# Performance work log

Hardware: AMD Instinct MI355X
Metric: run time of the kernel (lower is better)

Reference implementation:

```python
import jax, jax.numpy as jnp
import numpy as np

WS = 8            # window_size
N = WS * WS       # tokens per window = 64
C = 512           # dim
TEMB = 512        # temb_dim
H = 8             # num_heads
D = C // H        # head_dim = 64
B = 2048          # number of windows (batch * windows per image)


def _rel_pos_index(ws: int) -> np.ndarray:
    coords = np.stack(np.meshgrid(np.arange(ws), np.arange(ws), indexing='ij'))  # (2, ws, ws)
    flat = coords.reshape(2, -1)                      # (2, N)
    rel = flat[:, :, None] - flat[:, None, :]         # (2, N, N)
    rel = rel.transpose(1, 2, 0).copy()               # (N, N, 2)
    rel[:, :, 0] += ws - 1
    rel[:, :, 1] += ws - 1
    rel[:, :, 0] *= 2 * ws - 1
    return rel.sum(-1)                                # (N, N) int

_RP_INDEX = jnp.asarray(_rel_pos_index(WS))           # (N, N)


def setup_inputs() -> dict:
    key = jax.random.key(0)
    ks = jax.random.split(key, 8)
    std = 0.02
    return {
        'x': jax.random.normal(ks[0], (B, N, C), dtype=jnp.float32),
        'temb': jax.random.normal(ks[1], (B, TEMB), dtype=jnp.float32),
        'w_qkv': jax.random.normal(ks[2], (C, 3 * C), dtype=jnp.float32) * std,
        'b_qkv': jnp.zeros((3 * C,), dtype=jnp.float32),
        'w_qkv_t': jax.random.normal(ks[3], (TEMB, 3 * C), dtype=jnp.float32) * std,
        'w_proj': jax.random.normal(ks[4], (C, C), dtype=jnp.float32) * std,
        'b_proj': jnp.zeros((C,), dtype=jnp.float32),
        'rpb_table': jax.random.normal(ks[5], ((2 * WS - 1) ** 2, H), dtype=jnp.float32) * std,
    }


def reference(x, temb, w_qkv, b_qkv, w_qkv_t, w_proj, b_proj, rpb_table):
    # x: (B, N, C), temb: (B, TEMB)
    scale = D ** (-0.5)
    qkv = x @ w_qkv + b_qkv + (temb @ w_qkv_t)[:, None, :]     # (B, N, 3C)
    qkv = qkv.reshape(x.shape[0], N, 3, H, D)
    q = qkv[:, :, 0].transpose(0, 2, 1, 3)                      # (B, H, N, D)
    k = qkv[:, :, 1].transpose(0, 2, 1, 3)
    v = qkv[:, :, 2].transpose(0, 2, 1, 3)
    attn = jnp.einsum('bhnd,bhmd->bhnm', q * scale, k)          # (B, H, N, N)
    bias = rpb_table[_RP_INDEX]                                 # (N, N, H)
    attn = attn + bias.transpose(2, 0, 1)[None]                 # + (1, H, N, N)
    attn = jax.nn.softmax(attn, axis=-1)
    out = jnp.einsum('bhnm,bhmd->bhnd', attn, v)                # (B, H, N, D)
    out = out.transpose(0, 2, 1, 3).reshape(x.shape[0], N, C)   # (B, N, C)
    return out @ w_proj + b_proj
```

## Files before the change

### kernel.cpp

```cpp
#include <hip/hip_runtime.h>

typedef __bf16 bf16;
typedef __bf16 bf16x4 __attribute__((ext_vector_type(4)));
typedef __bf16 bf16x8 __attribute__((ext_vector_type(8)));
typedef float f32x4 __attribute__((ext_vector_type(4)));

#define MFMA(a, b, c) __builtin_amdgcn_mfma_f32_16x16x32_bf16((a), (b), (c), 0, 0, 0)

__global__ void transpose_cast(const float* __restrict__ in, bf16* __restrict__ out,
                               int R, int C) {
  int i = blockIdx.x * 256 + threadIdx.x;
  if (i >= R * C) return;
  int r = i / C, c = i - r * C;
  out[(size_t)c * R + r] = (bf16)in[i];
}

template <bool AF32>
__global__ __launch_bounds__(256) void gemm_bt_bias(
    const void* __restrict__ Ap, const bf16* __restrict__ Bt,
    const float* __restrict__ bias, float* __restrict__ C,
    int M, int N, int K) {
  __shared__ bf16 lA[128 * 32];
  __shared__ bf16 lB[128 * 32];
  const int t = threadIdx.x, l = t & 63;
  const int w = t >> 6, wr = w >> 1, wc = w & 1;
  const int li = l & 15, kl = (l >> 4) << 3;
  const long bm0 = (long)blockIdx.x * 128, bn0 = (long)blockIdx.y * 128;
  f32x4 acc[4][4] = {};
  for (int ks = 0; ks < (K >> 5); ++ks) {
    const int k0 = ks << 5;
    __syncthreads();
#pragma unroll
    for (int i = 0; i < 2; ++i) {
      int u = t + (i << 8);
      int row = u >> 2, kc = (u & 3) << 3;
      if constexpr (AF32) {
        const float* ag = (const float*)Ap + (bm0 + row) * K + k0 + kc;
        f32x4 v0 = *((const f32x4*)ag);
        f32x4 v1 = *((const f32x4*)(ag + 4));
        bf16x8 pk;
        pk[0] = (bf16)v0[0]; pk[1] = (bf16)v0[1]; pk[2] = (bf16)v0[2]; pk[3] = (bf16)v0[3];
        pk[4] = (bf16)v1[0]; pk[5] = (bf16)v1[1]; pk[6] = (bf16)v1[2]; pk[7] = (bf16)v1[3];
        *((bf16x8*)&lA[u << 3]) = pk;
      } else {
        *((bf16x8*)&lA[u << 3]) =
            *((const bf16x8*)((const bf16*)Ap + (bm0 + row) * K + k0 + kc));
      }
      *((bf16x8*)&lB[u << 3]) = *((const bf16x8*)&Bt[(bn0 + row) * K + k0 + kc]);
    }
    __syncthreads();
    bf16x8 af[4], bfr[4];
#pragma unroll
    for (int mt = 0; mt < 4; ++mt)
      af[mt] = *((const bf16x8*)&lA[(wr * 64 + mt * 16 + li) * 32 + kl]);
#pragma unroll
    for (int nt = 0; nt < 4; ++nt)
      bfr[nt] = *((const bf16x8*)&lB[(wc * 64 + nt * 16 + li) * 32 + kl]);
#pragma unroll
    for (int mt = 0; mt < 4; ++mt)
#pragma unroll
      for (int nt = 0; nt < 4; ++nt)
        acc[mt][nt] = MFMA(af[mt], bfr[nt], acc[mt][nt]);
  }
#pragma unroll
  for (int mt = 0; mt < 4; ++mt)
#pragma unroll
    for (int nt = 0; nt < 4; ++nt) {
      long col = bn0 + wc * 64 + nt * 16 + li;
      float bv = bias[col];
#pragma unroll
      for (int r = 0; r < 4; ++r) {
        long row = bm0 + wr * 64 + mt * 16 + ((l >> 4) << 2) + r;
        C[row * N + col] = acc[mt][nt][r] + bv;
      }
    }
}

__global__ __launch_bounds__(256) void fused_qkv_attn(
    const float* __restrict__ x, const bf16* __restrict__ w1t,
    const float* __restrict__ tbias, const float* __restrict__ rpb,
    bf16* __restrict__ attn_out) {
  __shared__ bf16 xs[64 * 520];
  __shared__ float ts[1536];
  __shared__ bf16 qs[64 * 72];
  __shared__ bf16 kts[64 * 72];
  __shared__ bf16 vts[64 * 72];
  __shared__ bf16 ps[64 * 72];

  const int b = blockIdx.x;
  const int t = threadIdx.x, l = t & 63, w = t >> 6;
  const int li = l & 15, lg = l >> 4, kl = lg << 3;

  {
    const float* xb = x + (size_t)b * (64 * 512);
#pragma unroll
    for (int i = 0; i < 32; ++i) {
      int f4 = t + (i << 8);
      int n = f4 >> 7, c4 = (f4 & 127) << 2;
      f32x4 v = *((const f32x4*)&xb[n * 512 + c4]);
      bf16x4 pk;
      pk[0] = (bf16)v[0]; pk[1] = (bf16)v[1]; pk[2] = (bf16)v[2]; pk[3] = (bf16)v[3];
      *((bf16x4*)&xs[n * 520 + c4]) = pk;
    }
    const float* tb = tbias + (size_t)b * 1536;
    for (int i = t; i < 1536; i += 256) ts[i] = tb[i];
  }

  int rpidx[4][4];
#pragma unroll
  for (int ct = 0; ct < 4; ++ct)
#pragma unroll
    for (int r = 0; r < 4; ++r) {
      int n = 16 * w + (lg << 2) + r, m = 16 * ct + li;
      rpidx[ct][r] = (((n >> 3) - (m >> 3) + 7) * 15 + ((n & 7) - (m & 7) + 7)) * 8;
    }
  __syncthreads();

  for (int h = 0; h < 8; ++h) {
    f32x4 acc[3][4] = {};
    int j0[3];
#pragma unroll
    for (int ct = 0; ct < 3; ++ct) {
      int lc = 48 * w + 16 * ct;
      j0[ct] = (lc >> 6) * 512 + h * 64 + (lc & 63);
    }
#pragma unroll 4
    for (int ks = 0; ks < 16; ++ks) {
      int k0 = ks << 5;
      bf16x8 af[4];
#pragma unroll
      for (int mt = 0; mt < 4; ++mt)
        af[mt] = *((const bf16x8*)&xs[(mt * 16 + li) * 520 + k0 + kl]);
#pragma unroll
      for (int ct = 0; ct < 3; ++ct) {
        bf16x8 bw = *((const bf16x8*)&w1t[(size_t)(j0[ct] + li) * 512 + k0 + kl]);
#pragma unroll
        for (int mt = 0; mt < 4; ++mt)
          acc[ct][mt] = MFMA(af[mt], bw, acc[ct][mt]);
      }
    }
#pragma unroll
    for (int ct = 0; ct < 3; ++ct) {
      int lc = 48 * w + 16 * ct;
      int sec = lc >> 6, dc = lc & 63;
      float tb = ts[j0[ct] + li];
#pragma unroll
      for (int mt = 0; mt < 4; ++mt) {
        int row0 = mt * 16 + (lg << 2);
        if (sec == 0) {
#pragma unroll
          for (int r = 0; r < 4; ++r)
            qs[(row0 + r) * 72 + dc + li] = (bf16)((acc[ct][mt][r] + tb) * 0.125f);
        } else if (sec == 1) {
#pragma unroll
          for (int r = 0; r < 4; ++r)
            kts[(row0 + r) * 72 + dc + li] = (bf16)(acc[ct][mt][r] + tb);
        } else {
          bf16x4 pk;
#pragma unroll
          for (int r = 0; r < 4; ++r) pk[r] = (bf16)(acc[ct][mt][r] + tb);
          *((bf16x4*)&vts[(dc + li) * 72 + row0]) = pk;
        }
      }
    }
    __syncthreads();

    f32x4 accS[4] = {};
#pragma unroll
    for (int kk = 0; kk < 2; ++kk) {
      bf16x8 aq = *((const bf16x8*)&qs[(16 * w + li) * 72 + kk * 32 + kl]);
#pragma unroll
      for (int ct = 0; ct < 4; ++ct) {
        bf16x8 bk = *((const bf16x8*)&kts[(16 * ct + li) * 72 + kk * 32 + kl]);
        accS[ct] = MFMA(aq, bk, accS[ct]);
      }
    }
    const float* rpbh = rpb + h;
    float sv[4][4], rsum[4];
#pragma unroll
    for (int ct = 0; ct < 4; ++ct)
#pragma unroll
      for (int r = 0; r < 4; ++r)
        sv[ct][r] = accS[ct][r] + rpbh[rpidx[ct][r]];
#pragma unroll
    for (int r = 0; r < 4; ++r) {
      float m = fmaxf(fmaxf(sv[0][r], sv[1][r]), fmaxf(sv[2][r], sv[3][r]));
      m = fmaxf(m, __shfl_xor(m, 1));
      m = fmaxf(m, __shfl_xor(m, 2));
      m = fmaxf(m, __shfl_xor(m, 4));
      m = fmaxf(m, __shfl_xor(m, 8));
      float s = 0.f;
#pragma unroll
      for (int ct = 0; ct < 4; ++ct) {
        float p = __expf(sv[ct][r] - m);
        sv[ct][r] = p;
        s += p;
      }
      s += __shfl_xor(s, 1);
      s += __shfl_xor(s, 2);
      s += __shfl_xor(s, 4);
      s += __shfl_xor(s, 8);
      rsum[r] = s;
    }
#pragma unroll
    for (int ct = 0; ct < 4; ++ct)
#pragma unroll
      for (int r = 0; r < 4; ++r)
        ps[(16 * w + (lg << 2) + r) * 72 + 16 * ct + li] = (bf16)sv[ct][r];

    f32x4 accO[4] = {};
#pragma unroll
    for (int kk = 0; kk < 2; ++kk) {
      bf16x8 ap = *((const bf16x8*)&ps[(16 * w + li) * 72 + kk * 32 + kl]);
#pragma unroll
      for (int ct = 0; ct < 4; ++ct) {
        bf16x8 bv = *((const bf16x8*)&vts[(16 * ct + li) * 72 + kk * 32 + kl]);
        accO[ct] = MFMA(ap, bv, accO[ct]);
      }
    }
    bf16* ob = attn_out + (size_t)b * (64 * 512) + h * 64;
    float rinv[4];
#pragma unroll
    for (int r = 0; r < 4; ++r) rinv[r] = 1.0f / rsum[r];
#pragma unroll
    for (int ct = 0; ct < 4; ++ct)
#pragma unroll
      for (int r = 0; r < 4; ++r)
        ob[(size_t)(16 * w + (lg << 2) + r) * 512 + 16 * ct + li] =
            (bf16)(accO[ct][r] * rinv[r]);
    __syncthreads();
  }
}

extern "C" void kernel_launch(void* const* d_in, const int* in_sizes, int n_in,
                              void* d_out, int out_size, void* d_ws, size_t ws_size,
                              hipStream_t stream) {
  (void)in_sizes; (void)n_in; (void)out_size; (void)ws_size;
  const float* x       = (const float*)d_in[0];
  const float* temb    = (const float*)d_in[1];
  const float* w_qkv   = (const float*)d_in[2];
  const float* b_qkv   = (const float*)d_in[3];
  const float* w_qkv_t = (const float*)d_in[4];
  const float* w_proj  = (const float*)d_in[5];
  const float* b_proj  = (const float*)d_in[6];
  const float* rpb     = (const float*)d_in[7];
  float* out = (float*)d_out;

  char* ws = (char*)d_ws;
  size_t off = 0;
  auto take = [&](size_t bytes) {
    void* p = ws + off;
    off += (bytes + 255) & ~(size_t)255;
    return p;
  };
  bf16* w1t  = (bf16*)take((size_t)1536 * 512 * 2);
  bf16* w3t  = (bf16*)take((size_t)1536 * 512 * 2);
  bf16* w2t  = (bf16*)take((size_t)512 * 512 * 2);
  float* tb  = (float*)take((size_t)2048 * 1536 * 4);
  bf16* attn = (bf16*)take((size_t)131072 * 512 * 2);

  transpose_cast<<<(512 * 1536 + 255) / 256, 256, 0, stream>>>(w_qkv, w1t, 512, 1536);
  transpose_cast<<<(512 * 1536 + 255) / 256, 256, 0, stream>>>(w_qkv_t, w3t, 512, 1536);
  transpose_cast<<<(512 * 512 + 255) / 256, 256, 0, stream>>>(w_proj, w2t, 512, 512);

  gemm_bt_bias<true><<<dim3(2048 / 128, 1536 / 128), 256, 0, stream>>>(
      temb, w3t, b_qkv, tb, 2048, 1536, 512);

  fused_qkv_attn<<<2048, 256, 0, stream>>>(x, w1t, tb, rpb, attn);

  gemm_bt_bias<false><<<dim3(131072 / 128, 512 / 128), 256, 0, stream>>>(
      attn, w2t, b_proj, out, 131072, 512, 512);
}
```

Before: 935.5 us.

## Process two heads per iteration with 512-thread blocks in fused attention

The fused QKV+attention kernel now launches 512 threads (8 waves) and handles two heads per loop iteration. The first four waves work on one head and the last four on the other, and Q/K/V shared buffers are doubled per head. The separate P buffer is removed and P is written back into the Q buffer. The aim is to halve the number of sequential head iterations and barriers, and to raise wave-level parallelism per block. The cost is more LDS per block, which may lower occupancy, and the in-place reuse of Q for P relies on ordering within a wave.

```diff
diff --git a/kernel.cpp b/kernel.cpp
--- a/kernel.cpp
+++ b/kernel.cpp
@@ -76,26 +76,26 @@
     }
 }
 
-__global__ __launch_bounds__(256) void fused_qkv_attn(
+__global__ __launch_bounds__(512) void fused_qkv_attn(
     const float* __restrict__ x, const bf16* __restrict__ w1t,
     const float* __restrict__ tbias, const float* __restrict__ rpb,
     bf16* __restrict__ attn_out) {
   __shared__ bf16 xs[64 * 520];
   __shared__ float ts[1536];
-  __shared__ bf16 qs[64 * 72];
-  __shared__ bf16 kts[64 * 72];
-  __shared__ bf16 vts[64 * 72];
-  __shared__ bf16 ps[64 * 72];
+  __shared__ bf16 qs[2][64 * 72];
+  __shared__ bf16 kts[2][64 * 72];
+  __shared__ bf16 vts[2][64 * 72];
 
   const int b = blockIdx.x;
   const int t = threadIdx.x, l = t & 63, w = t >> 6;
   const int li = l & 15, lg = l >> 4, kl = lg << 3;
+  const int strip = w & 3, hl = w >> 2;
 
   {
     const float* xb = x + (size_t)b * (64 * 512);
 #pragma unroll
-    for (int i = 0; i < 32; ++i) {
-      int f4 = t + (i << 8);
+    for (int i = 0; i < 16; ++i) {
+      int f4 = t + (i << 9);
       int n = f4 >> 7, c4 = (f4 & 127) << 2;
       f32x4 v = *((const f32x4*)&xb[n * 512 + c4]);
       bf16x4 pk;
@@ -103,7 +103,17 @@
       *((bf16x4*)&xs[n * 520 + c4]) = pk;
     }
     const float* tb = tbias + (size_t)b * 1536;
-    for (int i = t; i < 1536; i += 256) ts[i] = tb[i];
+    for (int i = t; i < 1536; i += 512) ts[i] = tb[i];
+  }
+
+  int chh[3], csec[3], cdc[3];
+#pragma unroll
+  for (int ct = 0; ct < 3; ++ct) {
+    int lc = 48 * w + 16 * ct;
+    int hh = lc >= 192;
+    chh[ct] = hh;
+    csec[ct] = (lc - 192 * hh) >> 6;
+    cdc[ct] = lc & 63;
   }
 
   int rpidx[4][4];
@@ -111,19 +121,17 @@
   for (int ct = 0; ct < 4; ++ct)
 #pragma unroll
     for (int r = 0; r < 4; ++r) {
-      int n = 16 * w + (lg << 2) + r, m = 16 * ct + li;
+      int n = 16 * strip + (lg << 2) + r, m = 16 * ct + li;
       rpidx[ct][r] = (((n >> 3) - (m >> 3) + 7) * 15 + ((n & 7) - (m & 7) + 7)) * 8;
     }
   __syncthreads();
 
-  for (int h = 0; h < 8; ++h) {
+  for (int hp = 0; hp < 4; ++hp) {
     f32x4 acc[3][4] = {};
     int j0[3];
 #pragma unroll
-    for (int ct = 0; ct < 3; ++ct) {
-      int lc = 48 * w + 16 * ct;
-      j0[ct] = (lc >> 6) * 512 + h * 64 + (lc & 63);
-    }
+    for (int ct = 0; ct < 3; ++ct)
+      j0[ct] = csec[ct] * 512 + (hp * 2 + chh[ct]) * 64 + cdc[ct];
 #pragma unroll 4
     for (int ks = 0; ks < 16; ++ks) {
       int k0 = ks << 5;
@@ -141,8 +149,7 @@
     }
 #pragma unroll
     for (int ct = 0; ct < 3; ++ct) {
-      int lc = 48 * w + 16 * ct;
-      int sec = lc >> 6, dc = lc & 63;
+      int hh = chh[ct], sec = csec[ct], dc = cdc[ct];
       float tb = ts[j0[ct] + li];
 #pragma unroll
       for (int mt = 0; mt < 4; ++mt) {
@@ -150,16 +157,16 @@
         if (sec == 0) {
 #pragma unroll
           for (int r = 0; r < 4; ++r)
-            qs[(row0 + r) * 72 + dc + li] = (bf16)((acc[ct][mt][r] + tb) * 0.125f);
+            qs[hh][(row0 + r) * 72 + dc + li] = (bf16)((acc[ct][mt][r] + tb) * 0.125f);
         } else if (sec == 1) {
 #pragma unroll
           for (int r = 0; r < 4; ++r)
-            kts[(row0 + r) * 72 + dc + li] = (bf16)(acc[ct][mt][r] + tb);
+            kts[hh][(row0 + r) * 72 + dc + li] = (bf16)(acc[ct][mt][r] + tb);
         } else {
           bf16x4 pk;
 #pragma unroll
           for (int r = 0; r < 4; ++r) pk[r] = (bf16)(acc[ct][mt][r] + tb);
-          *((bf16x4*)&vts[(dc + li) * 72 + row0]) = pk;
+          *((bf16x4*)&vts[hh][(dc + li) * 72 + row0]) = pk;
         }
       }
     }
@@ -168,13 +175,14 @@
     f32x4 accS[4] = {};
 #pragma unroll
     for (int kk = 0; kk < 2; ++kk) {
-      bf16x8 aq = *((const bf16x8*)&qs[(16 * w + li) * 72 + kk * 32 + kl]);
+      bf16x8 aq = *((const bf16x8*)&qs[hl][(16 * strip + li) * 72 + kk * 32 + kl]);
 #pragma unroll
       for (int ct = 0; ct < 4; ++ct) {
-        bf16x8 bk = *((const bf16x8*)&kts[(16 * ct + li) * 72 + kk * 32 + kl]);
+        bf16x8 bk = *((const bf16x8*)&kts[hl][(16 * ct + li) * 72 + kk * 32 + kl]);
         accS[ct] = MFMA(aq, bk, accS[ct]);
       }
     }
+    const int h = hp * 2 + hl;
     const float* rpbh = rpb + h;
     float sv[4][4], rsum[4];
 #pragma unroll
@@ -206,15 +214,15 @@
     for (int ct = 0; ct < 4; ++ct)
 #pragma unroll
       for (int r = 0; r < 4; ++r)
-        ps[(16 * w + (lg << 2) + r) * 72 + 16 * ct + li] = (bf16)sv[ct][r];
+        qs[hl][(16 * strip + (lg << 2) + r) * 72 + 16 * ct + li] = (bf16)sv[ct][r];
 
     f32x4 accO[4] = {};
 #pragma unroll
     for (int kk = 0; kk < 2; ++kk) {
-      bf16x8 ap = *((const bf16x8*)&ps[(16 * w + li) * 72 + kk * 32 + kl]);
+      bf16x8 ap = *((const bf16x8*)&qs[hl][(16 * strip + li) * 72 + kk * 32 + kl]);
 #pragma unroll
       for (int ct = 0; ct < 4; ++ct) {
-        bf16x8 bv = *((const bf16x8*)&vts[(16 * ct + li) * 72 + kk * 32 + kl]);
+        bf16x8 bv = *((const bf16x8*)&vts[hl][(16 * ct + li) * 72 + kk * 32 + kl]);
         accO[ct] = MFMA(ap, bv, accO[ct]);
       }
     }
@@ -226,7 +234,7 @@
     for (int ct = 0; ct < 4; ++ct)
 #pragma unroll
       for (int r = 0; r < 4; ++r)
-        ob[(size_t)(16 * w + (lg << 2) + r) * 512 + 16 * ct + li] =
+        ob[(size_t)(16 * strip + (lg << 2) + r) * 512 + 16 * ct + li] =
             (bf16)(accO[ct][r] * rinv[r]);
     __syncthreads();
   }
@@ -266,7 +274,7 @@
   gemm_bt_bias<true><<<dim3(2048 / 128, 1536 / 128), 256, 0, stream>>>(
       temb, w3t, b_qkv, tb, 2048, 1536, 512);
 
-  fused_qkv_attn<<<2048, 256, 0, stream>>>(x, w1t, tb, rpb, attn);
+  fused_qkv_attn<<<2048, 512, 0, stream>>>(x, w1t, tb, rpb, attn);
 
   gemm_bt_bias<false><<<dim3(131072 / 128, 512 / 128), 256, 0, stream>>>(
       attn, w2t, b_proj, out, 131072, 512, 512);
```

Measured after the change: 757.8 us. 1.23x faster.

## Split fused QKV-attention into tiled QKV GEMM plus per-window attention kernel

Applied to the files above, without the earlier changes.

Replaces the fused per-window kernel, which recomputed QKV by streaming weights from global memory for each head, with a 128x128 tiled GEMM that writes head-major Q/K/V (V transposed via swapped MFMA operands) into a bf16 workspace. A separate attention kernel double-buffers per-head Q/K/V tiles with global_load_lds and XOR-swizzled LDS, and writes its output in place over Q. The projection GEMM reads that head-blocked layout with direct-to-LDS loads and swizzling. This trades extra global round-trips of the QKV intermediate for better weight reuse and occupancy.

```diff
diff --git a/kernel.cpp b/kernel.cpp
--- a/kernel.cpp
+++ b/kernel.cpp
@@ -6,6 +6,15 @@
 typedef float f32x4 __attribute__((ext_vector_type(4)));
 
 #define MFMA(a, b, c) __builtin_amdgcn_mfma_f32_16x16x32_bf16((a), (b), (c), 0, 0, 0)
+
+constexpr size_t SEC = (size_t)2048 * 8 * 64 * 64;
+
+template <bool B> struct BC { static constexpr bool v = B; };
+
+__device__ __forceinline__ void gload16(const void* g, void* l) {
+  __builtin_amdgcn_global_load_lds((const __attribute__((address_space(1))) void*)g,
+                                   (__attribute__((address_space(3))) void*)l, 16, 0, 0);
+}
 
 __global__ void transpose_cast(const float* __restrict__ in, bf16* __restrict__ out,
                                int R, int C) {
@@ -15,9 +24,8 @@
   out[(size_t)c * R + r] = (bf16)in[i];
 }
 
-template <bool AF32>
-__global__ __launch_bounds__(256) void gemm_bt_bias(
-    const void* __restrict__ Ap, const bf16* __restrict__ Bt,
+__global__ __launch_bounds__(256) void gemm_temb(
+    const float* __restrict__ Ap, const bf16* __restrict__ Bt,
     const float* __restrict__ bias, float* __restrict__ C,
     int M, int N, int K) {
   __shared__ bf16 lA[128 * 32];
@@ -34,18 +42,13 @@
     for (int i = 0; i < 2; ++i) {
       int u = t + (i << 8);
       int row = u >> 2, kc = (u & 3) << 3;
-      if constexpr (AF32) {
-        const float* ag = (const float*)Ap + (bm0 + row) * K + k0 + kc;
-        f32x4 v0 = *((const f32x4*)ag);
-        f32x4 v1 = *((const f32x4*)(ag + 4));
-        bf16x8 pk;
-        pk[0] = (bf16)v0[0]; pk[1] = (bf16)v0[1]; pk[2] = (bf16)v0[2]; pk[3] = (bf16)v0[3];
-        pk[4] = (bf16)v1[0]; pk[5] = (bf16)v1[1]; pk[6] = (bf16)v1[2]; pk[7] = (bf16)v1[3];
-        *((bf16x8*)&lA[u << 3]) = pk;
-      } else {
-        *((bf16x8*)&lA[u << 3]) =
-            *((const bf16x8*)((const bf16*)Ap + (bm0 + row) * K + k0 + kc));
-      }
+      const float* ag = Ap + (bm0 + row) * K + k0 + kc;
+      f32x4 v0 = *((const f32x4*)ag);
+      f32x4 v1 = *((const f32x4*)(ag + 4));
+      bf16x8 pk;
+      pk[0] = (bf16)v0[0]; pk[1] = (bf16)v0[1]; pk[2] = (bf16)v0[2]; pk[3] = (bf16)v0[3];
+      pk[4] = (bf16)v1[0]; pk[5] = (bf16)v1[1]; pk[6] = (bf16)v1[2]; pk[7] = (bf16)v1[3];
+      *((bf16x8*)&lA[u << 3]) = pk;
       *((bf16x8*)&lB[u << 3]) = *((const bf16x8*)&Bt[(bn0 + row) * K + k0 + kc]);
     }
     __syncthreads();
@@ -76,35 +79,152 @@
     }
 }
 
-__global__ __launch_bounds__(256) void fused_qkv_attn(
-    const float* __restrict__ x, const bf16* __restrict__ w1t,
-    const float* __restrict__ tbias, const float* __restrict__ rpb,
-    bf16* __restrict__ attn_out) {
-  __shared__ bf16 xs[64 * 520];
-  __shared__ float ts[1536];
-  __shared__ bf16 qs[64 * 72];
-  __shared__ bf16 kts[64 * 72];
-  __shared__ bf16 vts[64 * 72];
-  __shared__ bf16 ps[64 * 72];
-
-  const int b = blockIdx.x;
-  const int t = threadIdx.x, l = t & 63, w = t >> 6;
-  const int li = l & 15, lg = l >> 4, kl = lg << 3;
-
-  {
-    const float* xb = x + (size_t)b * (64 * 512);
-#pragma unroll
-    for (int i = 0; i < 32; ++i) {
-      int f4 = t + (i << 8);
-      int n = f4 >> 7, c4 = (f4 & 127) << 2;
-      f32x4 v = *((const f32x4*)&xb[n * 512 + c4]);
-      bf16x4 pk;
-      pk[0] = (bf16)v[0]; pk[1] = (bf16)v[1]; pk[2] = (bf16)v[2]; pk[3] = (bf16)v[3];
-      *((bf16x4*)&xs[n * 520 + c4]) = pk;
-    }
-    const float* tb = tbias + (size_t)b * 1536;
-    for (int i = t; i < 1536; i += 256) ts[i] = tb[i];
+template <int MODE>
+__global__ __launch_bounds__(256) void mm128(
+    const void* __restrict__ Ap, const bf16* __restrict__ Bt,
+    const float* __restrict__ biasv, void* __restrict__ Cp) {
+  __shared__ bf16 lA[128 * 32];
+  __shared__ bf16 lB[128 * 32];
+  const int t = threadIdx.x, l = t & 63;
+  const int w = t >> 6, wr = w >> 1, wc = w & 1;
+  const int li = l & 15, lg = l >> 4;
+  const int bm0 = blockIdx.y * 128;
+  const int bnG = blockIdx.x * 128;
+  const bool isv = (MODE == 1) && (bnG >= 1024);
+  const int arow = t >> 1, acol = (t & 1) << 4;
+
+  f32x4 acc[4][4] = {};
+
+  auto kloop = [&](auto swc) {
+    constexpr bool SW = decltype(swc)::v;
+    f32x4 pf[4];
+    if (MODE == 1) {
+      const float* xg = (const float*)Ap + (size_t)(bm0 + arow) * 512 + acol;
+#pragma unroll
+      for (int j = 0; j < 4; ++j) pf[j] = *((const f32x4*)(xg + 4 * j));
+    }
+    for (int ks = 0; ks < 16; ++ks) {
+      const int k0 = ks << 5;
+      __syncthreads();
+      if (MODE == 1) {
+#pragma unroll
+        for (int j = 0; j < 2; ++j) {
+          bf16x8 pk;
+#pragma unroll
+          for (int e = 0; e < 4; ++e) {
+            pk[e] = (bf16)pf[2 * j][e];
+            pk[e + 4] = (bf16)pf[2 * j + 1][e];
+          }
+          int s = (acol >> 3) + j;
+          int p = s ^ ((arow >> 1) & 3);
+          *((bf16x8*)&lA[arow * 32 + p * 8]) = pk;
+        }
+      } else {
+#pragma unroll
+        for (int i = 0; i < 2; ++i) {
+          int u = t + (i << 8);
+          int row = u >> 2, p = u & 3;
+          int c0 = k0 + ((p ^ ((row >> 1) & 3)) << 3);
+          int gr = bm0 + row;
+          const bf16* src = (const bf16*)Ap +
+                            (((size_t)(gr >> 6) * 8 + (c0 >> 6)) << 12) +
+                            (gr & 63) * 64 + (c0 & 63);
+          gload16(src, &lA[(w * 64 + (i << 8)) * 8]);
+        }
+      }
+#pragma unroll
+      for (int i = 0; i < 2; ++i) {
+        int u = t + (i << 8);
+        int row = u >> 2, p = u & 3;
+        int c0 = k0 + ((p ^ ((row >> 1) & 3)) << 3);
+        gload16(Bt + (size_t)(bnG + row) * 512 + c0, &lB[(w * 64 + (i << 8)) * 8]);
+      }
+      __syncthreads();
+      if (MODE == 1 && ks < 15) {
+        const float* xg = (const float*)Ap + (size_t)(bm0 + arow) * 512 + k0 + 32 + acol;
+#pragma unroll
+        for (int j = 0; j < 4; ++j) pf[j] = *((const f32x4*)(xg + 4 * j));
+      }
+      bf16x8 af[4], bfr[4];
+#pragma unroll
+      for (int mt = 0; mt < 4; ++mt) {
+        int row = wr * 64 + mt * 16 + li;
+        af[mt] = *((const bf16x8*)&lA[row * 32 + ((lg ^ ((row >> 1) & 3)) << 3)]);
+      }
+#pragma unroll
+      for (int nt = 0; nt < 4; ++nt) {
+        int row = wc * 64 + nt * 16 + li;
+        bfr[nt] = *((const bf16x8*)&lB[row * 32 + ((lg ^ ((row >> 1) & 3)) << 3)]);
+      }
+#pragma unroll
+      for (int mt = 0; mt < 4; ++mt)
+#pragma unroll
+        for (int nt = 0; nt < 4; ++nt)
+          acc[mt][nt] = SW ? MFMA(bfr[nt], af[mt], acc[mt][nt])
+                           : MFMA(af[mt], bfr[nt], acc[mt][nt]);
+    }
+  };
+  if (isv) kloop(BC<true>{}); else kloop(BC<false>{});
+
+  if (MODE == 0) {
+    float* C = (float*)Cp;
+#pragma unroll
+    for (int nt = 0; nt < 4; ++nt) {
+      int col = bnG + wc * 64 + nt * 16 + li;
+      float bv = biasv[col];
+#pragma unroll
+      for (int mt = 0; mt < 4; ++mt) {
+        int row = bm0 + wr * 64 + mt * 16 + (lg << 2);
+#pragma unroll
+        for (int r = 0; r < 4; ++r)
+          C[(size_t)(row + r) * 512 + col] = acc[mt][nt][r] + bv;
+      }
+    }
+  } else if (!isv) {
+    bf16* qkv = (bf16*)Cp;
+    const int b = (bm0 >> 6) + wr;
+#pragma unroll
+    for (int nt = 0; nt < 4; ++nt) {
+      int col = bnG + wc * 64 + nt * 16 + li;
+      int sec = col >> 9, h = (col >> 6) & 7, d = col & 63;
+      float bv = biasv[(size_t)b * 1536 + col];
+      float sc = (sec == 0) ? 0.125f : 1.0f;
+      bf16* dst = qkv + (size_t)sec * SEC + (((size_t)b * 8 + h) << 12) + d;
+#pragma unroll
+      for (int mt = 0; mt < 4; ++mt) {
+        int n0 = mt * 16 + (lg << 2);
+#pragma unroll
+        for (int r = 0; r < 4; ++r)
+          dst[(n0 + r) * 64] = (bf16)((acc[mt][nt][r] + bv) * sc);
+      }
+    }
+  } else {
+    bf16* qkv = (bf16*)Cp;
+    const int b = (bm0 >> 6) + wr;
+#pragma unroll
+    for (int nt = 0; nt < 4; ++nt) {
+      int colb = bnG + wc * 64 + nt * 16 + (lg << 2);
+#pragma unroll
+      for (int r = 0; r < 4; ++r) {
+        int col = colb + r;
+        int h = (col >> 6) & 7, d = col & 63;
+        float bv = biasv[(size_t)b * 1536 + col];
+        bf16* dst = qkv + 2 * SEC + (((size_t)b * 8 + h) << 12) + d * 64;
+#pragma unroll
+        for (int mt = 0; mt < 4; ++mt) {
+          int n = mt * 16 + li;
+          dst[n] = (bf16)(acc[mt][nt][r] + bv);
+        }
+      }
+    }
   }
+}
+
+__global__ __launch_bounds__(256, 4) void attn_win(bf16* qkv,
+                                                   const float* __restrict__ rpb) {
+  __shared__ bf16 stg[2][3][4096];
+  const int b = blockIdx.x, t = threadIdx.x, l = t & 63, w = t >> 6;
+  const int li = l & 15, lg = l >> 4;
 
   int rpidx[4][4];
 #pragma unroll
@@ -114,64 +234,39 @@
       int n = 16 * w + (lg << 2) + r, m = 16 * ct + li;
       rpidx[ct][r] = (((n >> 3) - (m >> 3) + 7) * 15 + ((n & 7) - (m & 7) + 7)) * 8;
     }
-  __syncthreads();
-
+
+  auto stage = [&](int h, int buf) {
+#pragma unroll
+    for (int tt = 0; tt < 3; ++tt) {
+      const bf16* src = qkv + (size_t)tt * SEC + (((size_t)b * 8 + h) << 12);
+#pragma unroll
+      for (int i = 0; i < 2; ++i) {
+        int u = t + (i << 8);
+        int row = u >> 3, s = u & 7;
+        gload16(src + row * 64 + ((s ^ (row & 7)) << 3),
+                &stg[buf][tt][(w * 64 + (i << 8)) * 8]);
+      }
+    }
+  };
+
+  stage(0, 0);
   for (int h = 0; h < 8; ++h) {
-    f32x4 acc[3][4] = {};
-    int j0[3];
-#pragma unroll
-    for (int ct = 0; ct < 3; ++ct) {
-      int lc = 48 * w + 16 * ct;
-      j0[ct] = (lc >> 6) * 512 + h * 64 + (lc & 63);
-    }
-#pragma unroll 4
-    for (int ks = 0; ks < 16; ++ks) {
-      int k0 = ks << 5;
-      bf16x8 af[4];
-#pragma unroll
-      for (int mt = 0; mt < 4; ++mt)
-        af[mt] = *((const bf16x8*)&xs[(mt * 16 + li) * 520 + k0 + kl]);
-#pragma unroll
-      for (int ct = 0; ct < 3; ++ct) {
-        bf16x8 bw = *((const bf16x8*)&w1t[(size_t)(j0[ct] + li) * 512 + k0 + kl]);
-#pragma unroll
-        for (int mt = 0; mt < 4; ++mt)
-          acc[ct][mt] = MFMA(af[mt], bw, acc[ct][mt]);
-      }
-    }
-#pragma unroll
-    for (int ct = 0; ct < 3; ++ct) {
-      int lc = 48 * w + 16 * ct;
-      int sec = lc >> 6, dc = lc & 63;
-      float tb = ts[j0[ct] + li];
-#pragma unroll
-      for (int mt = 0; mt < 4; ++mt) {
-        int row0 = mt * 16 + (lg << 2);
-        if (sec == 0) {
-#pragma unroll
-          for (int r = 0; r < 4; ++r)
-            qs[(row0 + r) * 72 + dc + li] = (bf16)((acc[ct][mt][r] + tb) * 0.125f);
-        } else if (sec == 1) {
-#pragma unroll
-          for (int r = 0; r < 4; ++r)
-            kts[(row0 + r) * 72 + dc + li] = (bf16)(acc[ct][mt][r] + tb);
-        } else {
-          bf16x4 pk;
-#pragma unroll
-          for (int r = 0; r < 4; ++r) pk[r] = (bf16)(acc[ct][mt][r] + tb);
-          *((bf16x4*)&vts[(dc + li) * 72 + row0]) = pk;
-        }
-      }
-    }
+    const int buf = h & 1;
     __syncthreads();
+    if (h < 7) stage(h + 1, buf ^ 1);
+    bf16* Q = stg[buf][0];
+    const bf16* K = stg[buf][1];
+    const bf16* V = stg[buf][2];
 
     f32x4 accS[4] = {};
 #pragma unroll
     for (int kk = 0; kk < 2; ++kk) {
-      bf16x8 aq = *((const bf16x8*)&qs[(16 * w + li) * 72 + kk * 32 + kl]);
+      int row = 16 * w + li;
+      bf16x8 aq = *((const bf16x8*)&Q[row * 64 + (((kk * 4 + lg) ^ (row & 7)) << 3)]);
 #pragma unroll
       for (int ct = 0; ct < 4; ++ct) {
-        bf16x8 bk = *((const bf16x8*)&kts[(16 * ct + li) * 72 + kk * 32 + kl]);
+        int kr = 16 * ct + li;
+        bf16x8 bk = *((const bf16x8*)&K[kr * 64 + (((kk * 4 + lg) ^ (kr & 7)) << 3)]);
         accS[ct] = MFMA(aq, bk, accS[ct]);
       }
     }
@@ -205,30 +300,32 @@
 #pragma unroll
     for (int ct = 0; ct < 4; ++ct)
 #pragma unroll
+      for (int r = 0; r < 4; ++r) {
+        int row = 16 * w + (lg << 2) + r;
+        int col = 16 * ct + li;
+        Q[row * 64 + (((col >> 3) ^ (row & 7)) << 3) + (col & 7)] = (bf16)sv[ct][r];
+      }
+    f32x4 accO[4] = {};
+#pragma unroll
+    for (int kk = 0; kk < 2; ++kk) {
+      int row = 16 * w + li;
+      bf16x8 ap = *((const bf16x8*)&Q[row * 64 + (((kk * 4 + lg) ^ (row & 7)) << 3)]);
+#pragma unroll
+      for (int ct = 0; ct < 4; ++ct) {
+        int vr = 16 * ct + li;
+        bf16x8 bv = *((const bf16x8*)&V[vr * 64 + (((kk * 4 + lg) ^ (vr & 7)) << 3)]);
+        accO[ct] = MFMA(ap, bv, accO[ct]);
+      }
+    }
+    bf16* ob = qkv + (((size_t)b * 8 + h) << 12);
+    float rinv[4];
+#pragma unroll
+    for (int r = 0; r < 4; ++r) rinv[r] = 1.0f / rsum[r];
+#pragma unroll
+    for (int ct = 0; ct < 4; ++ct)
+#pragma unroll
       for (int r = 0; r < 4; ++r)
-        ps[(16 * w + (lg << 2) + r) * 72 + 16 * ct + li] = (bf16)sv[ct][r];
-
-    f32x4 accO[4] = {};
-#pragma unroll
-    for (int kk = 0; kk < 2; ++kk) {
-      bf16x8 ap = *((const bf16x8*)&ps[(16 * w + li) * 72 + kk * 32 + kl]);
-#pragma unroll
-      for (int ct = 0; ct < 4; ++ct) {
-        bf16x8 bv = *((const bf16x8*)&vts[(16 * ct + li) * 72 + kk * 32 + kl]);
-        accO[ct] = MFMA(ap, bv, accO[ct]);
-      }
-    }
-    bf16* ob = attn_out + (size_t)b * (64 * 512) + h * 64;
-    float rinv[4];
-#pragma unroll
-    for (int r = 0; r < 4; ++r) rinv[r] = 1.0f / rsum[r];
-#pragma unroll
-    for (int ct = 0; ct < 4; ++ct)
-#pragma unroll
-      for (int r = 0; r < 4; ++r)
-        ob[(size_t)(16 * w + (lg << 2) + r) * 512 + 16 * ct + li] =
-            (bf16)(accO[ct][r] * rinv[r]);
-    __syncthreads();
+        ob[(16 * w + (lg << 2) + r) * 64 + 16 * ct + li] = (bf16)(accO[ct][r] * rinv[r]);
   }
 }
 
@@ -257,17 +354,18 @@
   bf16* w3t  = (bf16*)take((size_t)1536 * 512 * 2);
   bf16* w2t  = (bf16*)take((size_t)512 * 512 * 2);
   float* tb  = (float*)take((size_t)2048 * 1536 * 4);
-  bf16* attn = (bf16*)take((size_t)131072 * 512 * 2);
+  bf16* qkv  = (bf16*)take(3 * SEC * 2);
 
   transpose_cast<<<(512 * 1536 + 255) / 256, 256, 0, stream>>>(w_qkv, w1t, 512, 1536);
   transpose_cast<<<(512 * 1536 + 255) / 256, 256, 0, stream>>>(w_qkv_t, w3t, 512, 1536);
   transpose_cast<<<(512 * 512 + 255) / 256, 256, 0, stream>>>(w_proj, w2t, 512, 512);
 
-  gemm_bt_bias<true><<<dim3(2048 / 128, 1536 / 128), 256, 0, stream>>>(
+  gemm_temb<<<dim3(2048 / 128, 1536 / 128), 256, 0, stream>>>(
       temb, w3t, b_qkv, tb, 2048, 1536, 512);
 
-  fused_qkv_attn<<<2048, 256, 0, stream>>>(x, w1t, tb, rpb, attn);
-
-  gemm_bt_bias<false><<<dim3(131072 / 128, 512 / 128), 256, 0, stream>>>(
-      attn, w2t, b_proj, out, 131072, 512, 512);
-}
+  mm128<1><<<dim3(12, 1024), 256, 0, stream>>>(x, w1t, tb, qkv);
+
+  attn_win<<<2048, 256, 0, stream>>>(qkv, rpb);
+
+  mm128<0><<<dim3(4, 1024), 256, 0, stream>>>(qkv, w2t, b_proj, out);
+}
```

Result: faster. 915.1 us (-2.2%).
